# Kernel tuning notes

Hardware: AMD Instinct MI355X
Metric: run time of the kernel (lower is better)

Reference implementation:

```python
import jax, jax.numpy as jnp
import numpy as np

B, N, DIM = 2, 2048, 2048
H, DH = 16, 128            # heads, dim_head; dim_inner = H*DH = 2048
SOFTCAP = 50.0
SCALE = DH ** -0.5


def setup_inputs() -> dict:
    key = jax.random.key(0)
    k1, k2, k3, k4 = jax.random.split(key, 4)
    s = 1.0 / np.sqrt(DIM)
    x = jax.random.normal(k1, (B, N, DIM), dtype=jnp.float32)
    w_qkv = jax.random.normal(k2, (DIM, 3 * H * DH), dtype=jnp.float32) * s
    w_gates = jax.random.normal(k3, (DIM, H), dtype=jnp.float32) * s
    w_out = jax.random.normal(k4, (H * DH, DIM), dtype=jnp.float32) * s
    return {"x": x, "w_qkv": w_qkv, "w_gates": w_gates, "w_out": w_out}


def reference(x, w_qkv, w_gates, w_out):
    b, n, _ = x.shape
    # to_qkv: Linear then 'b n (qkv h d) -> qkv b h n d'
    qkv = (x @ w_qkv).reshape(b, n, 3, H, DH).transpose(2, 0, 3, 1, 4)
    q, k, v = qkv[0], qkv[1], qkv[2]            # each [b, h, n, d]
    q = q * SCALE
    sim = jnp.einsum('bhid,bhjd->bhij', q, k)   # [b, h, n, n]
    sim = jnp.tanh(sim / SOFTCAP) * SOFTCAP     # softclamp
    mask_value = -jnp.finfo(sim.dtype).max
    causal_mask = jnp.triu(jnp.ones((n, n), dtype=bool), 1)
    sim = jnp.where(causal_mask, mask_value, sim)
    attn = jax.nn.softmax(sim, axis=-1)         # dropout = 0.0 (eval)
    out = jnp.einsum('bhij,bhjd->bhid', attn, v)
    # gating: 'b n h -> b h n 1' then sigmoid
    gates = jax.nn.sigmoid(x @ w_gates)         # [b, n, h]
    out = out * gates.transpose(0, 2, 1)[..., None]
    # to_out: 'b h n d -> b n (h d)' then Linear
    out = out.transpose(0, 2, 1, 3).reshape(b, n, H * DH) @ w_out
    return out
```

## Files before the change

### kernel.cpp

```cpp
#include <hip/hip_runtime.h>
#include <hip/hip_bf16.h>
#include <math.h>


typedef __attribute__((ext_vector_type(8))) __bf16 bf16x8;
typedef __attribute__((ext_vector_type(4))) __bf16 bf16x4;
typedef __attribute__((ext_vector_type(4))) float f32x4;

#define MFMA_BF16(a, b, c) __builtin_amdgcn_mfma_f32_16x16x32_bf16((a), (b), (c), 0, 0, 0)

#define NB 2
#define NSEQ 2048
#define NDIM 2048
#define NH 16
#define NDH 128
#define SCALE_Q 0.08838834764831845f

#define AS1 __attribute__((address_space(1)))
#define AS3 __attribute__((address_space(3)))
static __device__ __forceinline__ void gload_lds16(const void* g, void* l) {
  __builtin_amdgcn_global_load_lds((AS1 const void*)g, (AS3 void*)l, 16, 0, 0);
}

static __device__ __forceinline__ unsigned pack2_bf16(float a, float b) {
  unsigned short ua = __builtin_bit_cast(unsigned short, (__bf16)a);
  unsigned short ub = __builtin_bit_cast(unsigned short, (__bf16)b);
  return (unsigned)ua | ((unsigned)ub << 16);
}

__global__ __launch_bounds__(256) void cvt_bf16_kernel(const float* __restrict__ in,
                                                       __bf16* __restrict__ out) {
  int i = blockIdx.x * 256 + threadIdx.x;
  float4 v = reinterpret_cast<const float4*>(in)[i];
  bf16x4 o;
  o[0] = (__bf16)v.x; o[1] = (__bf16)v.y; o[2] = (__bf16)v.z; o[3] = (__bf16)v.w;
  reinterpret_cast<bf16x4*>(out)[i] = o;
}

__global__ __launch_bounds__(256) void transpose_cvt_kernel(const float* __restrict__ in,
                                                            __bf16* __restrict__ out,
                                                            int K, int C) {
  __shared__ float tile[32][33];
  int c0 = blockIdx.x * 32, k0 = blockIdx.y * 32;
  int t = threadIdx.x;
  int lc = t & 31, lr = t >> 5;
#pragma unroll
  for (int rr = 0; rr < 4; ++rr)
    tile[lr + rr * 8][lc] = in[(size_t)(k0 + lr + rr * 8) * C + c0 + lc];
  __syncthreads();
#pragma unroll
  for (int rr = 0; rr < 4; ++rr)
    out[(size_t)(c0 + lr + rr * 8) * K + k0 + lc] = (__bf16)tile[lc][lr + rr * 8];
}

struct Smem256 {
  __bf16 A[2][2][256][32];
  __bf16 B[2][2][256][32];
};

static __device__ __forceinline__ void stage_chunk(const __bf16* __restrict__ gbase,
                                                   __bf16* lds_half, int ks, int kt,
                                                   int w, int l2, int l3) {
#pragma unroll
  for (int j = 0; j < 2; ++j) {
    int rl = j * 128 + w * 16 + l2;
    int kg = l3 ^ ((rl >> 1) & 3);
    gload_lds16(gbase + (size_t)rl * 2048 + kt * 64 + ks * 32 + kg * 8,
                lds_half + (j * 128 + w * 16) * 32);
  }
}

#define FRAGP(Sbase, row) \
  ((const bf16x8*)((Sbase) + (row) * 32 + (g ^ (((row) >> 1) & 3)) * 8))

static __device__ __forceinline__ void gemm256_core(const __bf16* __restrict__ Abase,
                                                    const __bf16* __restrict__ Bbase,
                                                    Smem256* S, f32x4 (*acc)[4]) {
  int tid = threadIdx.x;
  int w = tid >> 6, lane = tid & 63;
  int ln15 = lane & 15, g = lane >> 4;
  int wr = w >> 2, wc = w & 3;
  int l2 = lane >> 2, l3 = lane & 3;

#pragma unroll
  for (int i = 0; i < 8; ++i)
#pragma unroll
    for (int j = 0; j < 4; ++j) acc[i][j] = (f32x4){0.f, 0.f, 0.f, 0.f};

  stage_chunk(Abase, &S->A[0][0][0][0], 0, 0, w, l2, l3);
  stage_chunk(Bbase, &S->B[0][0][0][0], 0, 0, w, l2, l3);
  stage_chunk(Abase, &S->A[0][1][0][0], 1, 0, w, l2, l3);
  stage_chunk(Bbase, &S->B[0][1][0][0], 1, 0, w, l2, l3);

  for (int t = 0; t < 32; ++t) {
    int bf = t & 1, tb = bf ^ 1;
    int ts = (t < 31) ? t + 1 : 31;
    const __bf16* SA0 = &S->A[bf][0][0][0];
    const __bf16* SB0 = &S->B[bf][0][0][0];
    const __bf16* SA1 = &S->A[bf][1][0][0];
    const __bf16* SB1 = &S->B[bf][1][0][0];
    bf16x8 af[4], bfr[4];
    stage_chunk(Abase, &S->A[tb][0][0][0], 0, ts, w, l2, l3);
    asm volatile("s_waitcnt vmcnt(6)" ::: "memory");
    __builtin_amdgcn_s_barrier();
    asm volatile("" ::: "memory");
#pragma unroll
    for (int nf = 0; nf < 4; ++nf) { int row = wc * 64 + nf * 16 + ln15; bfr[nf] = *FRAGP(SB0, row); }
#pragma unroll
    for (int mf = 0; mf < 4; ++mf) { int row = wr * 128 + mf * 16 + ln15; af[mf] = *FRAGP(SA0, row); }
    __builtin_amdgcn_s_setprio(1);
#pragma unroll
    for (int mf = 0; mf < 4; ++mf)
#pragma unroll
      for (int nf = 0; nf < 4; ++nf) acc[mf][nf] = MFMA_BF16(af[mf], bfr[nf], acc[mf][nf]);
    __builtin_amdgcn_s_setprio(0);
    stage_chunk(Bbase, &S->B[tb][0][0][0], 0, ts, w, l2, l3);
#pragma unroll
    for (int mf = 0; mf < 4; ++mf) { int row = wr * 128 + (mf + 4) * 16 + ln15; af[mf] = *FRAGP(SA0, row); }
    __builtin_amdgcn_s_setprio(1);
#pragma unroll
    for (int mf = 0; mf < 4; ++mf)
#pragma unroll
      for (int nf = 0; nf < 4; ++nf) acc[mf + 4][nf] = MFMA_BF16(af[mf], bfr[nf], acc[mf + 4][nf]);
    __builtin_amdgcn_s_setprio(0);
    stage_chunk(Abase, &S->A[tb][1][0][0], 1, ts, w, l2, l3);
    asm volatile("s_waitcnt vmcnt(6)" ::: "memory");
    __builtin_amdgcn_s_barrier();
    asm volatile("" ::: "memory");
#pragma unroll
    for (int nf = 0; nf < 4; ++nf) { int row = wc * 64 + nf * 16 + ln15; bfr[nf] = *FRAGP(SB1, row); }
#pragma unroll
    for (int mf = 0; mf < 4; ++mf) { int row = wr * 128 + mf * 16 + ln15; af[mf] = *FRAGP(SA1, row); }
    __builtin_amdgcn_s_setprio(1);
#pragma unroll
    for (int mf = 0; mf < 4; ++mf)
#pragma unroll
      for (int nf = 0; nf < 4; ++nf) acc[mf][nf] = MFMA_BF16(af[mf], bfr[nf], acc[mf][nf]);
    __builtin_amdgcn_s_setprio(0);
    stage_chunk(Bbase, &S->B[tb][1][0][0], 1, ts, w, l2, l3);
#pragma unroll
    for (int mf = 0; mf < 4; ++mf) { int row = wr * 128 + (mf + 4) * 16 + ln15; af[mf] = *FRAGP(SA1, row); }
    __builtin_amdgcn_s_setprio(1);
#pragma unroll
    for (int mf = 0; mf < 4; ++mf)
#pragma unroll
      for (int nf = 0; nf < 4; ++nf) acc[mf + 4][nf] = MFMA_BF16(af[mf], bfr[nf], acc[mf + 4][nf]);
    __builtin_amdgcn_s_setprio(0);
  }
  asm volatile("s_waitcnt vmcnt(0)" ::: "memory");
}

__global__ __launch_bounds__(512, 2) void gemm_qkv256(const __bf16* __restrict__ A,
                                                      const __bf16* __restrict__ Bt,
                                                      __bf16* __restrict__ qb,
                                                      __bf16* __restrict__ kb,
                                                      __bf16* __restrict__ vtb) {
  __shared__ __align__(1024) Smem256 S;
  int sblk = blockIdx.x;
  int wg = (sblk & 7) * 48 + (sblk >> 3);
  int m0 = (wg / 24) * 256;
  int n0 = (wg % 24) * 256;
  f32x4 acc[8][4];
  gemm256_core(A + (size_t)m0 * 2048, Bt + (size_t)n0 * 2048, &S, acc);

  int tid = threadIdx.x;
  int w = tid >> 6, lane = tid & 63;
  int ln15 = lane & 15, g = lane >> 4;
  int wr = w >> 2, wc = w & 3;
  int qkv = n0 >> 11;
  int nloc = n0 & 2047;
#pragma unroll
  for (int nf = 0; nf < 4; ++nf) {
    int ng = nloc + wc * 64 + nf * 16 + ln15;
    int h = ng >> 7, d = ng & 127;
#pragma unroll
    for (int mf = 0; mf < 8; ++mf)
#pragma unroll
      for (int rr = 0; rr < 4; ++rr) {
        int m = m0 + wr * 128 + mf * 16 + g * 4 + rr;
        int b = m >> 11, n = m & 2047;
        int bh = b * NH + h;
        float v = acc[mf][nf][rr];
        if (qkv == 0)
          qb[((size_t)bh * NSEQ + n) * NDH + d] = (__bf16)(v * SCALE_Q);
        else if (qkv == 1)
          kb[((size_t)bh * NSEQ + n) * NDH + d] = (__bf16)v;
        else
          vtb[((size_t)bh * NDH + d) * NSEQ + n] = (__bf16)v;
      }
  }
}

__global__ __launch_bounds__(512, 2) void gemm_out256(const __bf16* __restrict__ A,
                                                      const __bf16* __restrict__ Bt,
                                                      float* __restrict__ out) {
  __shared__ __align__(1024) Smem256 S;
  int sblk = blockIdx.x;
  int wg = (sblk & 7) * 16 + (sblk >> 3);
  int m0 = (wg >> 3) * 256;
  int n0 = (wg & 7) * 256;
  f32x4 acc[8][4];
  gemm256_core(A + (size_t)m0 * 2048, Bt + (size_t)n0 * 2048, &S, acc);

  int tid = threadIdx.x;
  int w = tid >> 6, lane = tid & 63;
  int ln15 = lane & 15, g = lane >> 4;
  int wr = w >> 2, wc = w & 3;
#pragma unroll
  for (int mf = 0; mf < 8; ++mf)
#pragma unroll
    for (int nf = 0; nf < 4; ++nf)
#pragma unroll
      for (int rr = 0; rr < 4; ++rr) {
        int m = m0 + wr * 128 + mf * 16 + g * 4 + rr;
        int c = n0 + wc * 64 + nf * 16 + ln15;
        out[(size_t)m * NDIM + c] = acc[mf][nf][rr];
      }
}

__global__ __launch_bounds__(256) void gates_kernel(const float* __restrict__ x,
                                                    const float* __restrict__ wg,
                                                    float* __restrict__ gates) {
  __shared__ float red[64];
  int row = blockIdx.x;
  int tid = threadIdx.x;
  float acc[16];
#pragma unroll
  for (int h = 0; h < 16; ++h) acc[h] = 0.f;
  const float* xr = x + (size_t)row * NDIM;
  for (int k = tid; k < NDIM; k += 256) {
    float xv = xr[k];
    const float* wr = wg + (size_t)k * NH;
#pragma unroll
    for (int h = 0; h < 16; ++h) acc[h] += xv * wr[h];
  }
  int w = tid >> 6, lane = tid & 63;
#pragma unroll
  for (int h = 0; h < 16; ++h) {
    float v = acc[h];
#pragma unroll
    for (int off = 32; off; off >>= 1) v += __shfl_down(v, off);
    if (lane == 0) red[w * 16 + h] = v;
  }
  __syncthreads();
  if (tid < 16) {
    float s = red[tid] + red[16 + tid] + red[32 + tid] + red[48 + tid];
    int b = row >> 11, n = row & 2047;
    gates[((size_t)(b * NH + tid)) * NSEQ + n] = 1.f / (1.f + expf(-s));
  }
}

static __device__ __forceinline__ void attn_tile(const __bf16* __restrict__ Kl,
                                                 const __bf16* __restrict__ Vl,
                                                 const bf16x8* qf, f32x4* acc_o,
                                                 float& m_r, float& l_r,
                                                 int j0, int q0s, bool diag,
                                                 int ln15, int g) {
  f32x4 accS[4];
#pragma unroll
  for (int jt = 0; jt < 4; ++jt) {
    accS[jt] = (f32x4){0.f, 0.f, 0.f, 0.f};
#pragma unroll
    for (int kc = 0; kc < 4; ++kc) {
      int row = jt * 16 + ln15;
      int bc = (kc * 64 + g * 16) ^ ((row & 7) << 4);
      bf16x8 kf = *reinterpret_cast<const bf16x8*>(Kl + row * 128 + (bc >> 1));
      accS[jt] = MFMA_BF16(kf, qf[kc], accS[jt]);
    }
  }
  float s[4][4];
  float mt = -3.0e38f;
#pragma unroll
  for (int jt = 0; jt < 4; ++jt)
#pragma unroll
    for (int r = 0; r < 4; ++r) {
      float y = fminf(fmaxf(accS[jt][r] * 0.02f, -15.f), 15.f);
      float e2 = __expf(2.f * y);
      float v = 50.f - 100.f / (e2 + 1.f);
      if (diag && (j0 + jt * 16 + g * 4 + r > q0s + ln15)) v = -3.0e38f;
      s[jt][r] = v;
      mt = fmaxf(mt, v);
    }
  mt = fmaxf(mt, __shfl_xor(mt, 16));
  mt = fmaxf(mt, __shfl_xor(mt, 32));
  float mn = fmaxf(m_r, mt);
  float sc = __expf(m_r - mn);
  float p[4][4];
  float ps = 0.f;
#pragma unroll
  for (int jt = 0; jt < 4; ++jt)
#pragma unroll
    for (int r = 0; r < 4; ++r) {
      float pv = __expf(s[jt][r] - mn);
      p[jt][r] = pv;
      ps += pv;
    }
  ps += __shfl_xor(ps, 16);
  ps += __shfl_xor(ps, 32);
  l_r = l_r * sc + ps;
  m_r = mn;
  float scr[4];
#pragma unroll
  for (int r = 0; r < 4; ++r) scr[r] = __shfl(sc, g * 4 + r);
#pragma unroll
  for (int d0 = 0; d0 < 8; ++d0)
#pragma unroll
    for (int r = 0; r < 4; ++r) acc_o[d0][r] *= scr[r];
  int lane_lo = ln15 + 32 * (g & 1);
  int lane_hi = lane_lo + 16;
#pragma unroll
  for (int c = 0; c < 2; ++c) {
    unsigned P0w0 = pack2_bf16(p[2 * c][0], p[2 * c][1]);
    unsigned P0w1 = pack2_bf16(p[2 * c][2], p[2 * c][3]);
    unsigned P1w0 = pack2_bf16(p[2 * c + 1][0], p[2 * c + 1][1]);
    unsigned P1w1 = pack2_bf16(p[2 * c + 1][2], p[2 * c + 1][3]);
    unsigned a0 = (unsigned)__shfl((int)P0w0, lane_lo);
    unsigned a1 = (unsigned)__shfl((int)P0w1, lane_lo);
    unsigned b0 = (unsigned)__shfl((int)P1w0, lane_lo);
    unsigned b1 = (unsigned)__shfl((int)P1w1, lane_lo);
    unsigned c0 = (unsigned)__shfl((int)P0w0, lane_hi);
    unsigned c1 = (unsigned)__shfl((int)P0w1, lane_hi);
    unsigned e0 = (unsigned)__shfl((int)P1w0, lane_hi);
    unsigned e1 = (unsigned)__shfl((int)P1w1, lane_hi);
    union { unsigned u[4]; bf16x8 v; } pu;
    pu.u[0] = (g < 2) ? a0 : b0;
    pu.u[1] = (g < 2) ? a1 : b1;
    pu.u[2] = (g < 2) ? c0 : e0;
    pu.u[3] = (g < 2) ? c1 : e1;
    bf16x8 pa = pu.v;
#pragma unroll
    for (int d0 = 0; d0 < 8; ++d0) {
      int d = d0 * 16 + ln15;
      int bc = (c * 64 + g * 16) ^ ((d & 7) << 4);
      bf16x8 vf = *reinterpret_cast<const bf16x8*>(Vl + d * 64 + (bc >> 1));
      acc_o[d0] = MFMA_BF16(pa, vf, acc_o[d0]);
    }
  }
}

__global__ __launch_bounds__(256) void attn_kernel(const __bf16* __restrict__ qb,
                                                   const __bf16* __restrict__ kb,
                                                   const __bf16* __restrict__ vtb,
                                                   const float* __restrict__ gates,
                                                   __bf16* __restrict__ og) {
  __shared__ __align__(1024) __bf16 Kl[64 * 128];
  __shared__ __align__(1024) __bf16 Vl[128 * 64];
  int tid = threadIdx.x;
  int w = tid >> 6, lane = tid & 63;
  int ln15 = lane & 15, g = lane >> 4;
  int bx = blockIdx.x;
  int lo = bx & 15, bh = bx >> 4;
  int hi = 31 - lo;
  const __bf16* qh = qb + (size_t)bh * NSEQ * NDH;
  const __bf16* kh = kb + (size_t)bh * NSEQ * NDH;
  const __bf16* vh = vtb + (size_t)bh * NDH * NSEQ;

  int q0h = hi * 64 + w * 16;
  int q0l = lo * 64 + w * 16;
  bf16x8 qfh[4], qfl[4];
#pragma unroll
  for (int kc = 0; kc < 4; ++kc) {
    qfh[kc] = *reinterpret_cast<const bf16x8*>(qh + (size_t)(q0h + ln15) * NDH + kc * 32 + g * 8);
    qfl[kc] = *reinterpret_cast<const bf16x8*>(qh + (size_t)(q0l + ln15) * NDH + kc * 32 + g * 8);
  }

  f32x4 acc_h[8], acc_l[8];
#pragma unroll
  for (int d0 = 0; d0 < 8; ++d0) {
    acc_h[d0] = (f32x4){0.f, 0.f, 0.f, 0.f};
    acc_l[d0] = (f32x4){0.f, 0.f, 0.f, 0.f};
  }
  float m_h = -3.0e38f, l_h = 0.f, m_l = -3.0e38f, l_l = 0.f;

  for (int t = 0; t <= hi; ++t) {
    int j0 = t * 64;
    __syncthreads();
#pragma unroll
    for (int i = 0; i < 4; ++i) {
      int gi = (i * 4 + w) * 64 + lane;
      int kr = gi >> 4, kcs = gi & 15;
      int kc_ = kcs ^ (kr & 7);
      gload_lds16(kh + (size_t)(j0 + kr) * NDH + kc_ * 8, &Kl[(i * 4 + w) * 512]);
      int vr = gi >> 3, vcs = gi & 7;
      int vc_ = vcs ^ (vr & 7);
      gload_lds16(vh + (size_t)vr * NSEQ + j0 + vc_ * 8, &Vl[(i * 4 + w) * 512]);
    }
    __syncthreads();
    attn_tile(Kl, Vl, qfh, acc_h, m_h, l_h, j0, q0h, t == hi, ln15, g);
    if (t <= lo)
      attn_tile(Kl, Vl, qfl, acc_l, m_l, l_l, j0, q0l, t == lo, ln15, g);
  }

  int b = bh >> 4, h = bh & 15;
#pragma unroll
  for (int set = 0; set < 2; ++set) {
    int q0s = set ? q0l : q0h;
    f32x4* acc = set ? acc_l : acc_h;
    float lr = set ? l_l : l_h;
    float lv[4], gv[4];
#pragma unroll
    for (int r = 0; r < 4; ++r) {
      lv[r] = __shfl(lr, g * 4 + r);
      int row = q0s + g * 4 + r;
      gv[r] = gates[(size_t)bh * NSEQ + row] / lv[r];
    }
#pragma unroll
    for (int d0 = 0; d0 < 8; ++d0)
#pragma unroll
      for (int r = 0; r < 4; ++r) {
        int row = q0s + g * 4 + r;
        og[((size_t)(b * NSEQ + row)) * NDIM + h * NDH + d0 * 16 + ln15] =
            (__bf16)(acc[d0][r] * gv[r]);
      }
  }
}

extern "C" void kernel_launch(void* const* d_in, const int* in_sizes, int n_in,
                              void* d_out, int out_size, void* d_ws, size_t ws_size,
                              hipStream_t stream) {
  const float* x = (const float*)d_in[0];
  const float* w_qkv = (const float*)d_in[1];
  const float* w_gates = (const float*)d_in[2];
  const float* w_out = (const float*)d_in[3];
  float* out = (float*)d_out;
  char* ws = (char*)d_ws;

  __bf16* x_bf   = (__bf16*)(ws + 0);
  __bf16* wqkv_t = (__bf16*)(ws + 16777216);
  __bf16* wout_t = (__bf16*)(ws + 41943040);
  __bf16* q_buf  = (__bf16*)(ws + 50331648);
  __bf16* k_buf  = (__bf16*)(ws + 67108864);
  __bf16* vt_buf = (__bf16*)(ws + 83886080);
  float*  gates  = (float*)(ws + 100663296);
  __bf16* attn_g = (__bf16*)(ws + 100925440);

  cvt_bf16_kernel<<<8192, 256, 0, stream>>>(x, x_bf);
  transpose_cvt_kernel<<<dim3(192, 64), 256, 0, stream>>>(w_qkv, wqkv_t, 2048, 6144);
  transpose_cvt_kernel<<<dim3(64, 64), 256, 0, stream>>>(w_out, wout_t, 2048, 2048);
  gemm_qkv256<<<384, 512, 0, stream>>>(x_bf, wqkv_t, q_buf, k_buf, vt_buf);
  gates_kernel<<<4096, 256, 0, stream>>>(x, w_gates, gates);
  attn_kernel<<<512, 256, 0, stream>>>(q_buf, k_buf, vt_buf, gates, attn_g);
  gemm_out256<<<128, 512, 0, stream>>>(attn_g, wout_t, out);
}
```

Before: 400.8 us.

## Double-buffer K/V tiles, fuse hi/lo tiles, drop online softmax max

K/V tiles are now double-buffered in LDS: the next tile's global-to-LDS loads are issued before computing the current one, so load latency can overlap compute. The hi and lo query tiles share each K/V fragment load in one fused routine, with MFMA sections raised in priority. Because softcap bounds scores to at most 50, the running max and rescaling are removed and a fixed offset of 12 is subtracted before exp, with the row-sum reduced across lanes once at the end. This removes per-tile max reductions, shuffles and accumulator rescaling, at the cost of double the LDS use and reliance on that fixed bound for numerical range.

Measured after the change: 364.2 us. 9.1% less time.

```diff
diff --git a/kernel.cpp b/kernel.cpp
--- a/kernel.cpp
+++ b/kernel.cpp
@@ -250,101 +250,99 @@
   }
 }
 
-static __device__ __forceinline__ void attn_tile(const __bf16* __restrict__ Kl,
-                                                 const __bf16* __restrict__ Vl,
-                                                 const bf16x8* qf, f32x4* acc_o,
-                                                 float& m_r, float& l_r,
-                                                 int j0, int q0s, bool diag,
-                                                 int ln15, int g) {
-  f32x4 accS[4];
+static __device__ __forceinline__ void softcap_p(const f32x4* accS, float (*p)[4],
+                                                 float& l_r, int j0, int q0s,
+                                                 bool diag, int ln15, int g) {
+#pragma unroll
+  for (int jt = 0; jt < 4; ++jt)
+#pragma unroll
+    for (int r = 0; r < 4; ++r) {
+      float e2 = __expf(accS[jt][r] * 0.04f);
+      float cap = 50.f - __fdividef(100.f, e2 + 1.f);
+      float pv = __expf(cap - 12.f);
+      if (diag && (j0 + jt * 16 + g * 4 + r > q0s + ln15)) pv = 0.f;
+      p[jt][r] = pv;
+      l_r += pv;
+    }
+}
+
+static __device__ __forceinline__ bf16x8 build_pa(const float (*p)[4], int c,
+                                                  int lane_lo, int lane_hi, int g) {
+  unsigned P0w0 = pack2_bf16(p[2 * c][0], p[2 * c][1]);
+  unsigned P0w1 = pack2_bf16(p[2 * c][2], p[2 * c][3]);
+  unsigned P1w0 = pack2_bf16(p[2 * c + 1][0], p[2 * c + 1][1]);
+  unsigned P1w1 = pack2_bf16(p[2 * c + 1][2], p[2 * c + 1][3]);
+  unsigned a0 = (unsigned)__shfl((int)P0w0, lane_lo);
+  unsigned a1 = (unsigned)__shfl((int)P0w1, lane_lo);
+  unsigned b0 = (unsigned)__shfl((int)P1w0, lane_lo);
+  unsigned b1 = (unsigned)__shfl((int)P1w1, lane_lo);
+  unsigned c0 = (unsigned)__shfl((int)P0w0, lane_hi);
+  unsigned c1 = (unsigned)__shfl((int)P0w1, lane_hi);
+  unsigned e0 = (unsigned)__shfl((int)P1w0, lane_hi);
+  unsigned e1 = (unsigned)__shfl((int)P1w1, lane_hi);
+  union { unsigned u[4]; bf16x8 v; } pu;
+  pu.u[0] = (g < 2) ? a0 : b0;
+  pu.u[1] = (g < 2) ? a1 : b1;
+  pu.u[2] = (g < 2) ? c0 : e0;
+  pu.u[3] = (g < 2) ? c1 : e1;
+  return pu.v;
+}
+
+static __device__ __forceinline__ void attn_tile2(const __bf16* __restrict__ Kl,
+                                                  const __bf16* __restrict__ Vl,
+                                                  const bf16x8* qfh, const bf16x8* qfl,
+                                                  f32x4* acc_h, f32x4* acc_l,
+                                                  float& l_h, float& l_l,
+                                                  int j0, int q0h, int q0l,
+                                                  bool diag_h, bool diag_l, bool do_lo,
+                                                  int ln15, int g) {
+  f32x4 sh[4], sl[4];
 #pragma unroll
   for (int jt = 0; jt < 4; ++jt) {
-    accS[jt] = (f32x4){0.f, 0.f, 0.f, 0.f};
+    sh[jt] = (f32x4){0.f, 0.f, 0.f, 0.f};
+    sl[jt] = (f32x4){0.f, 0.f, 0.f, 0.f};
+  }
+  __builtin_amdgcn_s_setprio(1);
+#pragma unroll
+  for (int jt = 0; jt < 4; ++jt)
 #pragma unroll
     for (int kc = 0; kc < 4; ++kc) {
       int row = jt * 16 + ln15;
       int bc = (kc * 64 + g * 16) ^ ((row & 7) << 4);
       bf16x8 kf = *reinterpret_cast<const bf16x8*>(Kl + row * 128 + (bc >> 1));
-      accS[jt] = MFMA_BF16(kf, qf[kc], accS[jt]);
-    }
-  }
-  float s[4][4];
-  float mt = -3.0e38f;
-#pragma unroll
-  for (int jt = 0; jt < 4; ++jt)
-#pragma unroll
-    for (int r = 0; r < 4; ++r) {
-      float y = fminf(fmaxf(accS[jt][r] * 0.02f, -15.f), 15.f);
-      float e2 = __expf(2.f * y);
-      float v = 50.f - 100.f / (e2 + 1.f);
-      if (diag && (j0 + jt * 16 + g * 4 + r > q0s + ln15)) v = -3.0e38f;
-      s[jt][r] = v;
-      mt = fmaxf(mt, v);
-    }
-  mt = fmaxf(mt, __shfl_xor(mt, 16));
-  mt = fmaxf(mt, __shfl_xor(mt, 32));
-  float mn = fmaxf(m_r, mt);
-  float sc = __expf(m_r - mn);
-  float p[4][4];
-  float ps = 0.f;
-#pragma unroll
-  for (int jt = 0; jt < 4; ++jt)
-#pragma unroll
-    for (int r = 0; r < 4; ++r) {
-      float pv = __expf(s[jt][r] - mn);
-      p[jt][r] = pv;
-      ps += pv;
-    }
-  ps += __shfl_xor(ps, 16);
-  ps += __shfl_xor(ps, 32);
-  l_r = l_r * sc + ps;
-  m_r = mn;
-  float scr[4];
-#pragma unroll
-  for (int r = 0; r < 4; ++r) scr[r] = __shfl(sc, g * 4 + r);
-#pragma unroll
-  for (int d0 = 0; d0 < 8; ++d0)
-#pragma unroll
-    for (int r = 0; r < 4; ++r) acc_o[d0][r] *= scr[r];
+      sh[jt] = MFMA_BF16(kf, qfh[kc], sh[jt]);
+      if (do_lo) sl[jt] = MFMA_BF16(kf, qfl[kc], sl[jt]);
+    }
+  __builtin_amdgcn_s_setprio(0);
+  float ph[4][4], pl[4][4];
+  softcap_p(sh, ph, l_h, j0, q0h, diag_h, ln15, g);
+  if (do_lo) softcap_p(sl, pl, l_l, j0, q0l, diag_l, ln15, g);
   int lane_lo = ln15 + 32 * (g & 1);
   int lane_hi = lane_lo + 16;
 #pragma unroll
   for (int c = 0; c < 2; ++c) {
-    unsigned P0w0 = pack2_bf16(p[2 * c][0], p[2 * c][1]);
-    unsigned P0w1 = pack2_bf16(p[2 * c][2], p[2 * c][3]);
-    unsigned P1w0 = pack2_bf16(p[2 * c + 1][0], p[2 * c + 1][1]);
-    unsigned P1w1 = pack2_bf16(p[2 * c + 1][2], p[2 * c + 1][3]);
-    unsigned a0 = (unsigned)__shfl((int)P0w0, lane_lo);
-    unsigned a1 = (unsigned)__shfl((int)P0w1, lane_lo);
-    unsigned b0 = (unsigned)__shfl((int)P1w0, lane_lo);
-    unsigned b1 = (unsigned)__shfl((int)P1w1, lane_lo);
-    unsigned c0 = (unsigned)__shfl((int)P0w0, lane_hi);
-    unsigned c1 = (unsigned)__shfl((int)P0w1, lane_hi);
-    unsigned e0 = (unsigned)__shfl((int)P1w0, lane_hi);
-    unsigned e1 = (unsigned)__shfl((int)P1w1, lane_hi);
-    union { unsigned u[4]; bf16x8 v; } pu;
-    pu.u[0] = (g < 2) ? a0 : b0;
-    pu.u[1] = (g < 2) ? a1 : b1;
-    pu.u[2] = (g < 2) ? c0 : e0;
-    pu.u[3] = (g < 2) ? c1 : e1;
-    bf16x8 pa = pu.v;
+    bf16x8 pah = build_pa(ph, c, lane_lo, lane_hi, g);
+    bf16x8 pal = build_pa(pl, c, lane_lo, lane_hi, g);
+    __builtin_amdgcn_s_setprio(1);
 #pragma unroll
     for (int d0 = 0; d0 < 8; ++d0) {
       int d = d0 * 16 + ln15;
       int bc = (c * 64 + g * 16) ^ ((d & 7) << 4);
       bf16x8 vf = *reinterpret_cast<const bf16x8*>(Vl + d * 64 + (bc >> 1));
-      acc_o[d0] = MFMA_BF16(pa, vf, acc_o[d0]);
-    }
-  }
-}
-
-__global__ __launch_bounds__(256) void attn_kernel(const __bf16* __restrict__ qb,
-                                                   const __bf16* __restrict__ kb,
-                                                   const __bf16* __restrict__ vtb,
-                                                   const float* __restrict__ gates,
-                                                   __bf16* __restrict__ og) {
-  __shared__ __align__(1024) __bf16 Kl[64 * 128];
-  __shared__ __align__(1024) __bf16 Vl[128 * 64];
+      acc_h[d0] = MFMA_BF16(pah, vf, acc_h[d0]);
+      if (do_lo) acc_l[d0] = MFMA_BF16(pal, vf, acc_l[d0]);
+    }
+    __builtin_amdgcn_s_setprio(0);
+  }
+}
+
+__global__ __launch_bounds__(256, 2) void attn_kernel(const __bf16* __restrict__ qb,
+                                                      const __bf16* __restrict__ kb,
+                                                      const __bf16* __restrict__ vtb,
+                                                      const float* __restrict__ gates,
+                                                      __bf16* __restrict__ og) {
+  __shared__ __align__(1024) __bf16 Kl[2][64 * 128];
+  __shared__ __align__(1024) __bf16 Vl[2][128 * 64];
   int tid = threadIdx.x;
   int w = tid >> 6, lane = tid & 63;
   int ln15 = lane & 15, g = lane >> 4;
@@ -370,26 +368,39 @@
     acc_h[d0] = (f32x4){0.f, 0.f, 0.f, 0.f};
     acc_l[d0] = (f32x4){0.f, 0.f, 0.f, 0.f};
   }
-  float m_h = -3.0e38f, l_h = 0.f, m_l = -3.0e38f, l_l = 0.f;
-
-  for (int t = 0; t <= hi; ++t) {
+  float l_h = 0.f, l_l = 0.f;
+
+  auto stage = [&](int t, int buf) {
     int j0 = t * 64;
-    __syncthreads();
 #pragma unroll
     for (int i = 0; i < 4; ++i) {
       int gi = (i * 4 + w) * 64 + lane;
       int kr = gi >> 4, kcs = gi & 15;
       int kc_ = kcs ^ (kr & 7);
-      gload_lds16(kh + (size_t)(j0 + kr) * NDH + kc_ * 8, &Kl[(i * 4 + w) * 512]);
+      gload_lds16(kh + (size_t)(j0 + kr) * NDH + kc_ * 8, &Kl[buf][(i * 4 + w) * 512]);
       int vr = gi >> 3, vcs = gi & 7;
       int vc_ = vcs ^ (vr & 7);
-      gload_lds16(vh + (size_t)vr * NSEQ + j0 + vc_ * 8, &Vl[(i * 4 + w) * 512]);
-    }
-    __syncthreads();
-    attn_tile(Kl, Vl, qfh, acc_h, m_h, l_h, j0, q0h, t == hi, ln15, g);
-    if (t <= lo)
-      attn_tile(Kl, Vl, qfl, acc_l, m_l, l_l, j0, q0l, t == lo, ln15, g);
-  }
+      gload_lds16(vh + (size_t)vr * NSEQ + j0 + vc_ * 8, &Vl[buf][(i * 4 + w) * 512]);
+    }
+  };
+
+  stage(0, 0);
+  for (int t = 0; t <= hi; ++t) {
+    int cb = t & 1;
+    if (t < hi) {
+      stage(t + 1, cb ^ 1);
+      asm volatile("s_waitcnt vmcnt(8)" ::: "memory");
+    } else {
+      asm volatile("s_waitcnt vmcnt(0)" ::: "memory");
+    }
+    __builtin_amdgcn_s_barrier();
+    attn_tile2(&Kl[cb][0], &Vl[cb][0], qfh, qfl, acc_h, acc_l, l_h, l_l,
+               t * 64, q0h, q0l, t == hi, t == lo, t <= lo, ln15, g);
+    __builtin_amdgcn_s_barrier();
+  }
+
+  l_h += __shfl_xor(l_h, 16); l_h += __shfl_xor(l_h, 32);
+  l_l += __shfl_xor(l_l, 16); l_l += __shfl_xor(l_l, 32);
 
   int b = bh >> 4, h = bh & 15;
 #pragma unroll
@@ -397,12 +408,12 @@
     int q0s = set ? q0l : q0h;
     f32x4* acc = set ? acc_l : acc_h;
     float lr = set ? l_l : l_h;
-    float lv[4], gv[4];
+    float gv[4];
 #pragma unroll
     for (int r = 0; r < 4; ++r) {
-      lv[r] = __shfl(lr, g * 4 + r);
+      float lv = __shfl(lr, g * 4 + r);
       int row = q0s + g * 4 + r;
-      gv[r] = gates[(size_t)bh * NSEQ + row] / lv[r];
+      gv[r] = gates[(size_t)bh * NSEQ + row] / lv;
     }
 #pragma unroll
     for (int d0 = 0; d0 < 8; ++d0)
```
